# Kernel optimization log

Hardware: AMD Instinct MI355X
Metric: run time of the kernel (lower is better)

## Reference

```python
import jax, jax.numpy as jnp
import numpy as np

B, S, H, F, E, TOPK = 4, 2048, 1024, 4096, 8, 2

def setup_inputs() -> dict:
    key = jax.random.key(0)
    ks = jax.random.split(key, 8)
    sh = 1.0 / np.sqrt(H)
    sf = 1.0 / np.sqrt(F)
    return {
        "hidden_states": jax.random.normal(ks[0], (B, S, H), jnp.float32),
        "Wr": jax.random.normal(ks[1], (H, E), jnp.float32) * sh,
        "br": jnp.zeros((E,), jnp.float32),
        "W1": jax.random.normal(ks[2], (E, H, F), jnp.float32) * sh,
        "b1": jax.random.normal(ks[3], (E, F), jnp.float32) * 0.01,
        "W2": jax.random.normal(ks[4], (E, F, H), jnp.float32) * sf,
        "b2": jax.random.normal(ks[5], (E, H), jnp.float32) * 0.01,
    }

def reference(hidden_states, Wr, br, W1, b1, W2, b2):
    b, s, h = hidden_states.shape
    x = hidden_states.reshape(-1, h)                      # [T, H]
    T = x.shape[0]
    logits = x @ Wr + br                                  # [T, E]
    routing_weights = jax.nn.softmax(logits, axis=-1)     # [T, E]
    top_v, top_i = jax.lax.top_k(logits, TOPK)            # [T, k]
    top_gates = jax.nn.softmax(top_v, axis=-1)            # [T, k]
    rows = jnp.arange(T)[:, None]
    dispatch = jnp.zeros((T, E), logits.dtype).at[rows, top_i].set(top_gates)  # [T, E]
    # Each expert runs densely on gate-scaled tokens: gelu((g*x)@W1 + b1)@W2 + b2.
    # (g*x)@W1 == g * (x@W1), so share the first GEMM across experts.
    z = jnp.einsum('th,ehf->etf', x, W1)                  # [E, T, F]
    a = jax.nn.gelu(dispatch.T[:, :, None] * z + b1[:, None, :], approximate=False)
    expert_out = jnp.einsum('etf,efh->eth', a, W2) + b2[:, None, :]  # [E, T, H]
    combined = jnp.einsum('te,eth->th', dispatch, expert_out)        # [T, H]
    final_output = combined.reshape(b, s, h)
    aux_loss = jnp.sum(routing_weights.mean(axis=0) * (dispatch.sum(axis=0) / T)) * E
    return (final_output,
            routing_weights.reshape(b, s, E),
            dispatch.reshape(b, s, E),
            aux_loss,
            logits.reshape(b, s, E))
```

## Files before the change

### kernel.cpp

```cpp
#include <hip/hip_runtime.h>

#define T_TOK 8192
#define H_DIM 1024
#define F_DIM 4096
#define E_NUM 8

typedef __attribute__((ext_vector_type(8))) short short8;
typedef __attribute__((ext_vector_type(4))) float f32x4;

__device__ __forceinline__ unsigned short f2bf(float f) {
  unsigned int u = __float_as_uint(f);
  return (unsigned short)((u + 0x7fffu + ((u >> 16) & 1u)) >> 16);
}

__device__ __forceinline__ float gelu_f(float v) {
  float z = 0.7978845608028654f * fmaf(0.044715f * v * v, v, v);
  z = fminf(fmaxf(z, -12.0f), 12.0f);
  const float ez = __expf(-2.0f * z);
  const float t = (1.0f - ez) / (1.0f + ez);
  return 0.5f * v * (1.0f + t);
}

__device__ __forceinline__ void gload16(const void* g, void* l) {
  __builtin_amdgcn_global_load_lds(
      (__attribute__((address_space(1))) const unsigned int*)(unsigned long long)g,
      (__attribute__((address_space(3))) unsigned int*)(unsigned int)(unsigned long long)l,
      16, 0, 0);
}

__global__ __launch_bounds__(256) void k_convert_x(const float* __restrict__ x,
                                                   unsigned short* __restrict__ xb) {
  int i = blockIdx.x * blockDim.x + threadIdx.x;
  float4 v = ((const float4*)x)[i];
  unsigned int lo = (unsigned int)f2bf(v.x) | ((unsigned int)f2bf(v.y) << 16);
  unsigned int hi = (unsigned int)f2bf(v.z) | ((unsigned int)f2bf(v.w) << 16);
  ((uint2*)xb)[i] = make_uint2(lo, hi);
}

__global__ __launch_bounds__(256) void k_transpose_cvt(const float* __restrict__ in,
                                                       unsigned short* __restrict__ out,
                                                       int R, int C) {
  __shared__ float tile[64][33];
  const size_t eoff = (size_t)blockIdx.z * R * C;
  const int c0 = blockIdx.x * 32, r0 = blockIdx.y * 64;
  const int tx = threadIdx.x & 31, ty = threadIdx.x >> 5;
#pragma unroll
  for (int i = 0; i < 8; ++i)
    tile[ty + i * 8][tx] = in[eoff + (size_t)(r0 + ty + i * 8) * C + (c0 + tx)];
  __syncthreads();
  const int ow = threadIdx.x & 63, oc = threadIdx.x >> 6;
#pragma unroll
  for (int i = 0; i < 8; ++i)
    out[eoff + (size_t)(c0 + oc + i * 4) * R + (r0 + ow)] = f2bf(tile[ow][oc + i * 4]);
}

__global__ __launch_bounds__(256) void k_logits(const float* __restrict__ x,
                                                const float* __restrict__ Wr,
                                                const float* __restrict__ br,
                                                double* __restrict__ ld,
                                                float* __restrict__ out_logits) {
  const int lane = threadIdx.x & 63;
  const int t = blockIdx.x * 4 + (threadIdx.x >> 6);
  double acc[8] = {0, 0, 0, 0, 0, 0, 0, 0};
#pragma unroll
  for (int i = 0; i < 16; ++i) {
    const int h = i * 64 + lane;
    const float xv = x[(size_t)t * H_DIM + h];
    const float4 wa = ((const float4*)Wr)[h * 2];
    const float4 wb = ((const float4*)Wr)[h * 2 + 1];
    acc[0] += (double)xv * wa.x; acc[1] += (double)xv * wa.y;
    acc[2] += (double)xv * wa.z; acc[3] += (double)xv * wa.w;
    acc[4] += (double)xv * wb.x; acc[5] += (double)xv * wb.y;
    acc[6] += (double)xv * wb.z; acc[7] += (double)xv * wb.w;
  }
#pragma unroll
  for (int e = 0; e < 8; ++e)
#pragma unroll
    for (int m = 32; m; m >>= 1) acc[e] += __shfl_xor(acc[e], m);
  if (lane == 0) {
#pragma unroll
    for (int e = 0; e < 8; ++e) {
      const double l = acc[e] + (double)br[e];
      ld[(size_t)t * 8 + e] = l;
      out_logits[(size_t)t * 8 + e] = (float)l;
    }
  }
}

__global__ __launch_bounds__(256) void k_decide(const double* __restrict__ ld,
                                                float* __restrict__ out_rw,
                                                float* __restrict__ out_disp,
                                                int* __restrict__ cnt,
                                                int* __restrict__ bidx,
                                                float* __restrict__ bgate,
                                                float* __restrict__ sums,
                                                int* __restrict__ slotmap) {
  __shared__ int hcnt[8];
  __shared__ int hbase[8];
  __shared__ float srw[8];
  __shared__ float sds[8];
  const int tloc = threadIdx.x;
  const int t = blockIdx.x * 256 + tloc;
  const int lane = tloc & 63;
  if (tloc < 8) { hcnt[tloc] = 0; srw[tloc] = 0.0f; sds[tloc] = 0.0f; }
  __syncthreads();

  double l[8];
#pragma unroll
  for (int e = 0; e < 8; ++e) l[e] = ld[(size_t)t * 8 + e];
  double mx = l[0];
#pragma unroll
  for (int e = 1; e < 8; ++e) mx = l[e] > mx ? l[e] : mx;
  double ex[8], se = 0.0;
#pragma unroll
  for (int e = 0; e < 8; ++e) { ex[e] = exp(l[e] - mx); se += ex[e]; }
  int i1 = 0;
#pragma unroll
  for (int e = 1; e < 8; ++e) if (l[e] > l[i1]) i1 = e;
  int i2 = (i1 == 0) ? 1 : 0;
#pragma unroll
  for (int e = 0; e < 8; ++e) if (e != i1 && l[e] > l[i2]) i2 = e;
  const double g1 = 1.0 / (1.0 + exp(l[i2] - l[i1]));
  const double g2 = 1.0 - g1;

  float rwv[8];
#pragma unroll
  for (int e = 0; e < 8; ++e) {
    rwv[e] = (float)(ex[e] / se);
    out_rw[(size_t)t * 8 + e] = rwv[e];
    out_disp[(size_t)t * 8 + e] = (e == i1) ? (float)g1 : (e == i2) ? (float)g2 : 0.0f;
  }
#pragma unroll
  for (int e = 0; e < 8; ++e) {
    float v = rwv[e];
#pragma unroll
    for (int m = 32; m; m >>= 1) v += __shfl_xor(v, m);
    if (lane == 0) atomicAdd(&srw[e], v);
  }
  atomicAdd(&sds[i1], (float)g1);
  atomicAdd(&sds[i2], (float)g2);

  const int loc1 = atomicAdd(&hcnt[i1], 1);
  const int loc2 = atomicAdd(&hcnt[i2], 1);
  __syncthreads();
  if (tloc < 8) hbase[tloc] = atomicAdd(&cnt[tloc], hcnt[tloc]);
  __syncthreads();
  const int s1 = hbase[i1] + loc1;
  const int s2 = hbase[i2] + loc2;
  bidx[i1 * T_TOK + s1] = t; bgate[i1 * T_TOK + s1] = (float)g1;
  bidx[i2 * T_TOK + s2] = t; bgate[i2 * T_TOK + s2] = (float)g2;
  slotmap[t * 2]     = (i1 << 16) | s1;
  slotmap[t * 2 + 1] = (i2 << 16) | s2;
  if (tloc < 8) {
    atomicAdd(&sums[tloc], srw[tloc]);
    atomicAdd(&sums[8 + tloc], sds[tloc]);
  }
}

__global__ void k_prefix_aux(const int* __restrict__ cnt, int* __restrict__ abase,
                             const float* __restrict__ sums, float* __restrict__ out_aux) {
  if (threadIdx.x == 0) {
    int base = 0;
    for (int e = 0; e < 8; ++e) { abase[e] = base; base += (cnt[e] + 127) & ~127; }
    abase[8] = base;
    double aux = 0.0;
    for (int e = 0; e < 8; ++e) aux += ((double)sums[e] / 8192.0) * ((double)sums[8 + e] / 8192.0);
    *out_aux = (float)(aux * 8.0);
  }
}

__global__ __launch_bounds__(256) void k_gemm1(
    const unsigned short* __restrict__ xb, const unsigned short* __restrict__ w1t,
    const float* __restrict__ b1, const int* __restrict__ bidx,
    const float* __restrict__ bgate, const int* __restrict__ abase,
    unsigned short* __restrict__ abuf) {
  const int e = blockIdx.z, by = blockIdx.y, bx = blockIdx.x;
  const int pb = abase[e];
  const int pcnt = abase[e + 1] - pb;
  if (by * 128 >= pcnt) return;
  const int tid = threadIdx.x, wid = tid >> 6, lane = tid & 63;
  const int r0 = tid >> 2, kseg = tid & 3;
  const int t0 = bidx[e * T_TOK + by * 128 + r0];
  const int t1 = bidx[e * T_TOK + by * 128 + 64 + r0];
  const char* gA0 = (const char*)(xb + (size_t)t0 * H_DIM + kseg * 8);
  const char* gA1 = (const char*)(xb + (size_t)t1 * H_DIM + kseg * 8);
  const char* gB0 = (const char*)(w1t + ((size_t)e * F_DIM + bx * 128 + r0) * H_DIM + kseg * 8);
  const char* gB1 = gB0 + (size_t)64 * H_DIM * 2;
  __shared__ __align__(16) char smem[2][16384];
  f32x4 acc[4][4] = {};
  const int wm = wid >> 1, wn = wid & 1;
  const int aoff = (wm * 64 + (lane & 15)) * 64 + (lane >> 4) * 16;
  const int boff = 8192 + (wn * 64 + (lane & 15)) * 64 + (lane >> 4) * 16;
  {
    char* s = smem[0] + wid * 1024;
    gload16(gA0, s); gload16(gA1, s + 4096);
    gload16(gB0, s + 8192); gload16(gB1, s + 12288);
  }
  __syncthreads();
  for (int kt = 0; kt < 32; ++kt) {
    const int cur = kt & 1;
    if (kt + 1 < 32) {
      const int koff = (kt + 1) * 64;
      char* s = smem[cur ^ 1] + wid * 1024;
      gload16(gA0 + koff, s); gload16(gA1 + koff, s + 4096);
      gload16(gB0 + koff, s + 8192); gload16(gB1 + koff, s + 12288);
    }
    short8 af[4], bf[4];
#pragma unroll
    for (int mi = 0; mi < 4; ++mi) af[mi] = *(const short8*)(smem[cur] + aoff + mi * 1024);
#pragma unroll
    for (int ni = 0; ni < 4; ++ni) bf[ni] = *(const short8*)(smem[cur] + boff + ni * 1024);
#pragma unroll
    for (int mi = 0; mi < 4; ++mi)
#pragma unroll
      for (int ni = 0; ni < 4; ++ni)
        acc[mi][ni] = __builtin_amdgcn_mfma_f32_16x16x32_bf16(af[mi], bf[ni], acc[mi][ni], 0, 0, 0);
    __syncthreads();
  }
  const int lcol = lane & 15, lr4 = (lane >> 4) * 4;
  const int gcol0 = bx * 128 + wn * 64;
  float b1v[4];
#pragma unroll
  for (int ni = 0; ni < 4; ++ni) b1v[ni] = b1[(size_t)e * F_DIM + gcol0 + ni * 16 + lcol];
  const float* bg_e = bgate + e * T_TOK + by * 128 + wm * 64;
  char* wsm = (char*)smem + wid * 8192;
#pragma unroll
  for (int mi = 0; mi < 4; ++mi) {
#pragma unroll
    for (int r = 0; r < 4; ++r) {
      const int wrow = mi * 16 + lr4 + r;
      const float gt = (by * 128 + wm * 64 + wrow < pcnt) ? bg_e[wrow] : 0.0f;
#pragma unroll
      for (int ni = 0; ni < 4; ++ni) {
        const float v = fmaf(gt, acc[mi][ni][r], b1v[ni]);
        const int col2 = (ni * 16 + lcol) * 2;
        *(unsigned short*)(wsm + wrow * 128 + (col2 ^ ((wrow & 7) << 4))) = f2bf(gelu_f(v));
      }
    }
  }
#pragma unroll
  for (int r = 0; r < 8; ++r) {
    const int row = r * 8 + (lane >> 3);
    const int chunk = (lane & 7) ^ (row & 7);
    const int grow = by * 128 + wm * 64 + row;
    if (grow < pcnt) {
      short8 vv = *(const short8*)(wsm + row * 128 + chunk * 16);
      *(short8*)(abuf + (size_t)(pb + grow) * F_DIM + gcol0 + (lane & 7) * 8) = vv;
    }
  }
}

#define MFMA_Q(qm_, qn_, Bset_)                                                        \
  do {                                                                                 \
    _Pragma("unroll") for (int kh = 0; kh < 2; ++kh)                                   \
    _Pragma("unroll") for (int mi = 0; mi < 4; ++mi)                                   \
    _Pragma("unroll") for (int ni = 0; ni < 2; ++ni)                                   \
      acc[(qm_)*4 + mi][(qn_)*2 + ni] = __builtin_amdgcn_mfma_f32_16x16x32_bf16(       \
          Areg[mi][kh], Bset_[ni][kh], acc[(qm_)*4 + mi][(qn_)*2 + ni], 0, 0, 0);      \
  } while (0)

#define LOAD_A(mh_)                                                                    \
  do {                                                                                 \
    const char* Ab = smem + slot * 65536 + (mh_)*16384;                                \
    _Pragma("unroll") for (int mi = 0; mi < 4; ++mi) {                                 \
      Areg[mi][0] = *(const short8*)(Ab + mi * 2048 + aoffk0);                         \
      Areg[mi][1] = *(const short8*)(Ab + mi * 2048 + aoffk1);                         \
    }                                                                                  \
  } while (0)

#define LOAD_B(set_, nh_)                                                              \
  do {                                                                                 \
    const char* Bb = smem + slot * 65536 + 32768 + (nh_)*16384;                        \
    _Pragma("unroll") for (int ni = 0; ni < 2; ++ni) {                                 \
      set_[ni][0] = *(const short8*)(Bb + ni * 2048 + boffk0);                         \
      set_[ni][1] = *(const short8*)(Bb + ni * 2048 + boffk1);                         \
    }                                                                                  \
  } while (0)

#define PHASE_TAIL(MFMA_STMT)                                                          \
  __builtin_amdgcn_s_barrier();                                                        \
  __builtin_amdgcn_s_setprio(1);                                                       \
  MFMA_STMT;                                                                           \
  __builtin_amdgcn_s_setprio(0);                                                       \
  __builtin_amdgcn_s_barrier();

__global__ __launch_bounds__(512, 2) void k_gemm2(
    const unsigned short* __restrict__ abuf, const unsigned short* __restrict__ w2t,
    const float* __restrict__ b2, const float* __restrict__ bgate,
    const int* __restrict__ abase, float* __restrict__ eout_a,
    float* __restrict__ eout_b, int split) {
  const int ez = blockIdx.z;
  const int e = ez & 7, ks = ez >> 3;
  const int by = blockIdx.y, bx = blockIdx.x;
  const int pb = abase[e], pcnt = abase[e + 1] - pb;
  if (by * 256 >= pcnt) return;
  const int g0 = ks * 32;
  const int gend = split ? (g0 + 32) : 64;
  float* eo = ks ? eout_b : eout_a;
  __shared__ char smem[131072];
  const int tid = threadIdx.x, wid = tid >> 6, lane = tid & 63;
  const int wr = wid >> 2, wc = wid & 3;
  const int rr0 = tid >> 3;
  const int kbyte = ((tid & 7) ^ (rr0 & 7)) * 16;
  const int d0 = tid * 16, d1 = d0 + 8192;
  const int aoffk0 = (wr * 64 + (lane & 15)) * 128 + (((lane >> 4) ^ (lane & 7)) * 16);
  const int aoffk1 = aoffk0 ^ 64;
  const int boffk0 = (wc * 32 + (lane & 15)) * 128 + (((lane >> 4) ^ (lane & 7)) * 16);
  const int boffk1 = boffk0 ^ 64;

  const char* Abase = (const char*)(abuf + (size_t)(pb + by * 256) * F_DIM);
  const int brB0 = ((rr0 >> 5) * 64 + (rr0 & 31));
  const char* Bbase = (const char*)(w2t + (size_t)e * H_DIM * F_DIM + (size_t)(bx * 256) * F_DIM);

#define G2_STAGE_A(g_, mh_)                                                            \
  do {                                                                                 \
    const char* s0 = Abase + (size_t)((mh_)*64 + rr0) * 8192 + (g_)*128 + kbyte;       \
    const char* s1 = Abase + (size_t)(128 + (mh_)*64 + rr0) * 8192 + (g_)*128 + kbyte; \
    char* dst = smem + (((g_)&1) * 65536) + (mh_)*16384;                               \
    gload16(s0, dst + d0); gload16(s1, dst + d1);                                      \
  } while (0)

#define G2_STAGE_B(g_, nh_)                                                            \
  do {                                                                                 \
    const char* s0 = Bbase + (size_t)(brB0 + (nh_)*32) * 8192 + (g_)*128 + kbyte;      \
    const char* s1 = Bbase + (size_t)(brB0 + 128 + (nh_)*32) * 8192 + (g_)*128 + kbyte;\
    char* dst = smem + (((g_)&1) * 65536) + 32768 + (nh_)*16384;                       \
    gload16(s0, dst + d0); gload16(s1, dst + d1);                                      \
  } while (0)

  f32x4 acc[8][4] = {};
  short8 Areg[4][2], B0reg[2][2], B1reg[2][2];

  G2_STAGE_A(g0, 0); G2_STAGE_B(g0, 1); G2_STAGE_A(g0, 1); G2_STAGE_B(g0, 0);
  G2_STAGE_A(g0 + 1, 0); G2_STAGE_B(g0 + 1, 1); G2_STAGE_A(g0 + 1, 1);
  asm volatile("s_waitcnt vmcnt(6)" ::: "memory");
  __builtin_amdgcn_sched_barrier(0);
  __builtin_amdgcn_s_barrier();

  for (int g = g0; g < gend; ++g) {
    const int slot = g & 1;
    LOAD_A(0); LOAD_B(B0reg, 0);
    if (g + 1 < gend) G2_STAGE_B(g + 1, 0);
    PHASE_TAIL(MFMA_Q(0, 0, B0reg));
    LOAD_B(B1reg, 1);
    if (g + 2 < gend) G2_STAGE_A(g + 2, 0);
    PHASE_TAIL(MFMA_Q(0, 1, B1reg));
    LOAD_A(1);
    if (g + 2 < gend) G2_STAGE_B(g + 2, 1);
    PHASE_TAIL(MFMA_Q(1, 1, B1reg));
    if (g + 2 < gend) {
      G2_STAGE_A(g + 2, 1);
      asm volatile("s_waitcnt vmcnt(6)" ::: "memory");
    } else if (g + 1 < gend) {
      asm volatile("s_waitcnt vmcnt(0)" ::: "memory");
    }
    __builtin_amdgcn_sched_barrier(0);
    PHASE_TAIL(MFMA_Q(1, 0, B0reg));
  }

  const int lcol = lane & 15;
  const int gcol0 = bx * 256 + wc * 64;
  float b2v[4];
#pragma unroll
  for (int n = 0; n < 4; ++n)
    b2v[n] = (ks == 0) ? b2[(size_t)e * H_DIM + gcol0 + n * 16 + lcol] : 0.0f;
  const float* bg_e = bgate + e * T_TOK;
#pragma unroll
  for (int m = 0; m < 8; ++m) {
    const int rl = wr * 128 + m * 16 + (lane >> 4) * 4;
#pragma unroll
    for (int j = 0; j < 4; ++j) {
      const int gm = by * 256 + rl + j;
      if (gm < pcnt) {
        const float gt = bg_e[gm];
        float* orow = eo + (size_t)(pb + gm) * H_DIM + gcol0;
#pragma unroll
        for (int n = 0; n < 4; ++n)
          orow[n * 16 + lcol] = (acc[m][n][j] + b2v[n]) * gt;
      }
    }
  }
#undef G2_STAGE_A
#undef G2_STAGE_B
}

__global__ __launch_bounds__(256) void k_combine(const float* __restrict__ ea,
                                                 const float* __restrict__ eb,
                                                 const int* __restrict__ slotmap,
                                                 const int* __restrict__ abase,
                                                 float* __restrict__ outf, int split) {
  const int t = blockIdx.x;
  const int c = threadIdx.x;
  const int v0 = slotmap[t * 2], v1 = slotmap[t * 2 + 1];
  const size_t row0 = (size_t)(abase[v0 >> 16] + (v0 & 0xffff)) * H_DIM;
  const size_t row1 = (size_t)(abase[v1 >> 16] + (v1 & 0xffff)) * H_DIM;
  float4 a = ((const float4*)(ea + row0))[c];
  float4 b = ((const float4*)(ea + row1))[c];
  float rx = a.x + b.x, ry = a.y + b.y, rz = a.z + b.z, rw = a.w + b.w;
  if (split) {
    float4 p = ((const float4*)(eb + row0))[c];
    float4 q = ((const float4*)(eb + row1))[c];
    rx += p.x + q.x; ry += p.y + q.y; rz += p.z + q.z; rw += p.w + q.w;
  }
  ((float4*)outf)[(size_t)t * 256 + c] = make_float4(rx, ry, rz, rw);
}

extern "C" void kernel_launch(void* const* d_in, const int* in_sizes, int n_in,
                              void* d_out, int out_size, void* d_ws, size_t ws_size,
                              hipStream_t stream) {
  const float* x  = (const float*)d_in[0];
  const float* Wr = (const float*)d_in[1];
  const float* br = (const float*)d_in[2];
  const float* W1 = (const float*)d_in[3];
  const float* b1 = (const float*)d_in[4];
  const float* W2 = (const float*)d_in[5];
  const float* b2 = (const float*)d_in[6];
  float* out = (float*)d_out;
  float* out_final  = out;
  float* out_rw     = out + 8388608;
  float* out_disp   = out_rw + 65536;
  float* out_aux    = out_disp + 65536;
  float* out_logits = out_aux + 1;

  char* ws = (char*)d_ws;
  unsigned short* xb   = (unsigned short*)(ws);
  unsigned short* w1t  = (unsigned short*)(ws + 16777216);
  unsigned short* w2t  = (unsigned short*)(ws + 83886080);
  unsigned short* abuf = (unsigned short*)(ws + 150994944);
  int*    bidx  = (int*)(ws + 293601280);
  float*  bgate = (float*)(ws + 293863424);
  int*    cnt   = (int*)(ws + 294125568);
  int*    abase = (int*)(ws + 294125632);
  float*  sums  = (float*)(ws + 294125696);
  double* ld    = (double*)(ws + 294125824);
  int*    slotmap = (int*)(ws + 294650112);
  float*  eout_a = (float*)(ws);
  float*  eout_b = (float*)(ws + 294715648);

  const int split = (ws_size >= (size_t)294715648 + 71303168) ? 1 : 0;

  hipMemsetAsync(cnt, 0, 64, stream);
  hipMemsetAsync(sums, 0, 64, stream);
  hipMemsetAsync(bidx, 0, 262144, stream);
  hipMemsetAsync(bgate, 0, 262144, stream);

  k_convert_x<<<8192, 256, 0, stream>>>(x, xb);
  k_transpose_cvt<<<dim3(128, 16, 8), 256, 0, stream>>>(W1, w1t, H_DIM, F_DIM);
  k_transpose_cvt<<<dim3(32, 64, 8), 256, 0, stream>>>(W2, w2t, F_DIM, H_DIM);
  k_logits<<<2048, 256, 0, stream>>>(x, Wr, br, ld, out_logits);
  k_decide<<<32, 256, 0, stream>>>(ld, out_rw, out_disp, cnt, bidx, bgate, sums, slotmap);
  k_prefix_aux<<<1, 64, 0, stream>>>(cnt, abase, sums, out_aux);
  k_gemm1<<<dim3(32, 24, 8), 256, 0, stream>>>(xb, w1t, b1, bidx, bgate, abase, abuf);
  k_gemm2<<<dim3(4, 32, split ? 16 : 8), 512, 0, stream>>>(abuf, w2t, b2, bgate, abase,
                                                           eout_a, eout_b, split);
  k_combine<<<8192, 256, 0, stream>>>(eout_a, eout_b, slotmap, abase, out_final, split);
}
```

Measured before the change: 552.4 us.

## Fuse x bf16 conversion into logits kernel and XCD-swizzle GEMM block order

The bf16 conversion of x now happens inside the logits kernel, which already reads x, so the separate conversion kernel and its extra pass over x are removed. Both expert GEMMs switch to a 1D grid with an XCD-aware swizzle (bid&7 striding) so that consecutive tiles of the same expert land on the same chiplet and share L2. GEMM2 also caps the token-row blocks at 12 instead of 32 in the split path, assuming per-expert padded counts never exceed 12×256 rows. That cap risks dropping tokens if routing is very skewed.

```diff
diff --git a/kernel.cpp b/kernel.cpp
--- a/kernel.cpp
+++ b/kernel.cpp
@@ -26,15 +26,6 @@
       (__attribute__((address_space(1))) const unsigned int*)(unsigned long long)g,
       (__attribute__((address_space(3))) unsigned int*)(unsigned int)(unsigned long long)l,
       16, 0, 0);
-}
-
-__global__ __launch_bounds__(256) void k_convert_x(const float* __restrict__ x,
-                                                   unsigned short* __restrict__ xb) {
-  int i = blockIdx.x * blockDim.x + threadIdx.x;
-  float4 v = ((const float4*)x)[i];
-  unsigned int lo = (unsigned int)f2bf(v.x) | ((unsigned int)f2bf(v.y) << 16);
-  unsigned int hi = (unsigned int)f2bf(v.z) | ((unsigned int)f2bf(v.w) << 16);
-  ((uint2*)xb)[i] = make_uint2(lo, hi);
 }
 
 __global__ __launch_bounds__(256) void k_transpose_cvt(const float* __restrict__ in,
@@ -58,7 +49,8 @@
                                                 const float* __restrict__ Wr,
                                                 const float* __restrict__ br,
                                                 double* __restrict__ ld,
-                                                float* __restrict__ out_logits) {
+                                                float* __restrict__ out_logits,
+                                                unsigned short* __restrict__ xb) {
   const int lane = threadIdx.x & 63;
   const int t = blockIdx.x * 4 + (threadIdx.x >> 6);
   double acc[8] = {0, 0, 0, 0, 0, 0, 0, 0};
@@ -66,6 +58,7 @@
   for (int i = 0; i < 16; ++i) {
     const int h = i * 64 + lane;
     const float xv = x[(size_t)t * H_DIM + h];
+    xb[(size_t)t * H_DIM + h] = f2bf(xv);
     const float4 wa = ((const float4*)Wr)[h * 2];
     const float4 wb = ((const float4*)Wr)[h * 2 + 1];
     acc[0] += (double)xv * wa.x; acc[1] += (double)xv * wa.y;
@@ -174,7 +167,12 @@
     const float* __restrict__ b1, const int* __restrict__ bidx,
     const float* __restrict__ bgate, const int* __restrict__ abase,
     unsigned short* __restrict__ abuf) {
-  const int e = blockIdx.z, by = blockIdx.y, bx = blockIdx.x;
+  const int bid = blockIdx.x;
+  const int swz = (bid & 7) * 768 + (bid >> 3);
+  const int bx = swz & 31;
+  const int r_ = swz >> 5;
+  const int by = r_ % 24;
+  const int e = r_ / 24;
   const int pb = abase[e];
   const int pcnt = abase[e + 1] - pb;
   if (by * 128 >= pcnt) return;
@@ -289,9 +287,19 @@
     const float* __restrict__ b2, const float* __restrict__ bgate,
     const int* __restrict__ abase, float* __restrict__ eout_a,
     float* __restrict__ eout_b, int split) {
-  const int ez = blockIdx.z;
-  const int e = ez & 7, ks = ez >> 3;
-  const int by = blockIdx.y, bx = blockIdx.x;
+  int e, ks, by, bx;
+  if (split) {
+    const int bid = blockIdx.x;
+    const int swz = (bid & 7) * 96 + (bid >> 3);
+    bx = swz & 3;
+    const int r_ = swz >> 2;
+    by = r_ % 12;
+    const int r2 = r_ / 12;
+    e = r2 & 7;
+    ks = r2 >> 3;
+  } else {
+    e = blockIdx.z & 7; ks = 0; by = blockIdx.y; bx = blockIdx.x;
+  }
   const int pb = abase[e], pcnt = abase[e + 1] - pb;
   if (by * 256 >= pcnt) return;
   const int g0 = ks * 32;
@@ -444,14 +452,16 @@
   hipMemsetAsync(bidx, 0, 262144, stream);
   hipMemsetAsync(bgate, 0, 262144, stream);
 
-  k_convert_x<<<8192, 256, 0, stream>>>(x, xb);
   k_transpose_cvt<<<dim3(128, 16, 8), 256, 0, stream>>>(W1, w1t, H_DIM, F_DIM);
   k_transpose_cvt<<<dim3(32, 64, 8), 256, 0, stream>>>(W2, w2t, F_DIM, H_DIM);
-  k_logits<<<2048, 256, 0, stream>>>(x, Wr, br, ld, out_logits);
+  k_logits<<<2048, 256, 0, stream>>>(x, Wr, br, ld, out_logits, xb);
   k_decide<<<32, 256, 0, stream>>>(ld, out_rw, out_disp, cnt, bidx, bgate, sums, slotmap);
   k_prefix_aux<<<1, 64, 0, stream>>>(cnt, abase, sums, out_aux);
-  k_gemm1<<<dim3(32, 24, 8), 256, 0, stream>>>(xb, w1t, b1, bidx, bgate, abase, abuf);
-  k_gemm2<<<dim3(4, 32, split ? 16 : 8), 512, 0, stream>>>(abuf, w2t, b2, bgate, abase,
-                                                           eout_a, eout_b, split);
+  k_gemm1<<<6144, 256, 0, stream>>>(xb, w1t, b1, bidx, bgate, abase, abuf);
+  if (split) {
+    k_gemm2<<<768, 512, 0, stream>>>(abuf, w2t, b2, bgate, abase, eout_a, eout_b, 1);
+  } else {
+    k_gemm2<<<dim3(4, 32, 8), 512, 0, stream>>>(abuf, w2t, b2, bgate, abase, eout_a, eout_b, 0);
+  }
   k_combine<<<8192, 256, 0, stream>>>(eout_a, eout_b, slotmap, abase, out_final, split);
 }
```

Measured after the change: 558.0 us. No clear change (+1.0%).
